# Optimization experiments

Hardware: AMD Instinct MI355X
Metric: run time of the kernel (lower is better)

## Reference

```python
import jax, jax.numpy as jnp
import numpy as np

# Dims derived from module build() with d_model=256
D_MODEL = 256
EXPAND = 2
D_STATE = 16
K_CONV = 4
CHUNK = 64
HEADDIM = 64
D_INNER = EXPAND * D_MODEL            # 512
NHEADS = D_INNER // HEADDIM           # 8
CONV_DIM = D_INNER + 2 * D_STATE      # 544
D_IN_PROJ = 3 * D_INNER + 2 * D_STATE + NHEADS  # 1576
BATCH, SEQ = 4, 4096


def setup_inputs() -> dict:
    key = jax.random.key(0)
    ks = jax.random.split(key, 11)
    def rn(k, shape, s=1.0):
        return jax.random.normal(k, shape, dtype=jnp.float32) * s
    return {
        "x": rn(ks[0], (BATCH, SEQ, D_MODEL)),
        "W_in": rn(ks[1], (D_MODEL, D_IN_PROJ), D_MODEL ** -0.5),
        "conv_w": rn(ks[2], (K_CONV, CONV_DIM), 0.3),
        "conv_b": rn(ks[3], (CONV_DIM,), 0.1),
        "A_log": rn(ks[4], (NHEADS, 2), 0.5),
        "dt_bias": rn(ks[5], (NHEADS,), 0.1),
        "D": rn(ks[6], (2 * NHEADS, 1), 0.5),
        "init_conv_state": rn(ks[7], (1, K_CONV, CONV_DIM), 0.1),
        "init_ssm_state": rn(ks[8], (1, 1, NHEADS, HEADDIM, D_STATE, 2), 0.1),
        "norm_w": rn(ks[9], (2 * D_INNER,), 0.5),
        "W_out": rn(ks[10], (2 * D_INNER, D_MODEL), (2 * D_INNER) ** -0.5),
    }


def _exp_segsum(a):
    # a: (..., T) complex. Returns exp(segsum(a)): lower-triangular (incl. diag)
    # with entry [i,j] = exp(sum_{j<d<=i} a_d), zero strictly above the diagonal.
    T = a.shape[-1]
    cs = jnp.cumsum(a, axis=-1)
    seg = cs[..., :, None] - cs[..., None, :]
    mask = jnp.tril(jnp.ones((T, T), dtype=bool))
    seg = jnp.where(mask, seg, 0.0)  # keep exp finite / grad-safe off-band
    return jnp.where(mask, jnp.exp(seg), 0.0)


def reference(x, W_in, conv_w, conv_b, A_log, dt_bias, D, init_conv_state,
              init_ssm_state, norm_w, W_out):
    b, L, _ = x.shape
    zxbcdt = x @ W_in  # (b, L, 3*d_inner + 2*d_state + nheads)
    z = zxbcdt[..., : 2 * D_INNER]
    xBC = zxbcdt[..., 2 * D_INNER: 3 * D_INNER + 2 * D_STATE]
    dt_raw = zxbcdt[..., 3 * D_INNER + 2 * D_STATE:]
    # dt scalar in call is 1/30, then *30 -> net factor 1
    dt = jnp.clip(jnp.exp(dt_raw + dt_bias), 0.0, 6.0)  # (b, L, h)

    # causal depthwise conv1d with learned initial conv state, relu6 activation
    prefix = jnp.broadcast_to(init_conv_state, (b, K_CONV, CONV_DIM))
    full = jnp.concatenate([prefix, xBC], axis=1)  # (b, K_CONV + L, conv_dim)
    conv = conv_b + sum(conv_w[j] * full[:, 1 + j: 1 + j + L] for j in range(K_CONV))
    xBC = jnp.clip(conv, 0.0, 6.0)  # relu6, last L of the L+1 valid outputs

    xin = xBC[..., :D_INNER]
    Bm = xBC[..., D_INNER: D_INNER + D_STATE].astype(jnp.complex64)
    Cm = xBC[..., D_INNER + D_STATE:].astype(jnp.complex64)
    xh = xin.reshape(b, L, NHEADS, HEADDIM).astype(jnp.complex64)

    A = -jnp.exp(A_log[:, 0]) + 1j * A_log[:, 1]  # (h,) complex
    dtc = dt.astype(jnp.complex64)
    Adt = A * dtc              # (b, L, h)
    xdt = xh * dtc[..., None]  # (b, L, h, p)

    # ---- chunked SSD (Mamba2-style) with complex state ----
    c = L // CHUNK
    xc = xdt.reshape(b, c, CHUNK, NHEADS, HEADDIM)
    Ac = Adt.reshape(b, c, CHUNK, NHEADS).transpose(0, 3, 1, 2)  # (b, h, c, l)
    Bc = Bm.reshape(b, c, CHUNK, D_STATE)
    Cc = Cm.reshape(b, c, CHUNK, D_STATE)

    A_cum = jnp.cumsum(Ac, axis=-1)          # (b, h, c, l)
    Lmat = _exp_segsum(Ac)                   # (b, h, c, l, l)
    Y_diag = jnp.einsum('bcln,bcsn,bhcls,bcshp->bclhp', Cc, Bc, Lmat, xc)

    decay_states = jnp.exp(A_cum[..., -1:] - A_cum)  # (b, h, c, l)
    states = jnp.einsum('bcln,bhcl,bclhp->bchpn', Bc, decay_states, xc)

    init_stat = init_ssm_state[:, 0, ..., 0] + 1j * init_ssm_state[:, 0, ..., 1]
    init_stat = jnp.broadcast_to(init_stat, (b, NHEADS, HEADDIM, D_STATE))[:, None]
    states = jnp.concatenate([init_stat, states], axis=1)  # (b, c+1, h, p, n)

    decay_chunk = _exp_segsum(jnp.pad(A_cum[..., -1], ((0, 0), (0, 0), (1, 0))))
    new_states = jnp.einsum('bhzc,bchpn->bzhpn', decay_chunk, states)
    Y_off = jnp.einsum('bcln,bchpn,bhcl->bclhp', Cc, new_states[:, :-1], jnp.exp(A_cum))

    Y = (Y_diag + Y_off).reshape(b, L, NHEADS, HEADDIM)  # complex

    # 'b l h p c -> b l (h c) p' : interleave real/imag per head
    y2 = jnp.stack([Y.real, Y.imag], axis=3).reshape(b, L, 2 * NHEADS, HEADDIM)
    xr = xin.reshape(b, L, NHEADS, HEADDIM)
    x2 = jnp.stack([xr, jnp.zeros_like(xr)], axis=3).reshape(b, L, 2 * NHEADS, HEADDIM)
    y2 = y2 + x2 * D  # D: (2h, 1) broadcasts over p
    y3 = y2.reshape(b, L, 2 * D_INNER)

    # RMSNorm gated by relu6(z)
    yz = y3 * jnp.clip(z, 0.0, 6.0)
    y4 = yz * jax.lax.rsqrt(jnp.mean(yz * yz, axis=-1, keepdims=True) + 1e-5) * norm_w
    return y4 @ W_out
```

## Files before the change

kernel.cpp:

```cpp
#include <hip/hip_runtime.h>
#include <math.h>

#define BATCHN 4
#define SEQL   4096
#define DMODEL 256
#define DIP    1576
#define DINNER 512
#define DZCOLS 1024
#define CONVD  544
#define NHEADS 8
#define HDIM   64
#define DSTATE 16
#define CHK    64
#define NCHUNK 64
#define MROWS  (BATCHN*SEQL)
#define NPAD   1664

typedef _Float16 half8 __attribute__((ext_vector_type(8)));
typedef short    s16x8 __attribute__((ext_vector_type(8)));
typedef float    f32x4 __attribute__((ext_vector_type(4)));

__device__ __forceinline__ float clip6f(float x) { return fminf(fmaxf(x, 0.0f), 6.0f); }

__global__ __launch_bounds__(256) void k_cvt_x(const float* __restrict__ X,
                                               _Float16* __restrict__ A)
{
    const int gid = blockIdx.x * 256 + threadIdx.x;
    const float4 a = *reinterpret_cast<const float4*>(X + (size_t)gid * 8);
    const float4 b = *reinterpret_cast<const float4*>(X + (size_t)gid * 8 + 4);
    half8 h;
    h[0] = (_Float16)a.x; h[1] = (_Float16)a.y; h[2] = (_Float16)a.z; h[3] = (_Float16)a.w;
    h[4] = (_Float16)b.x; h[5] = (_Float16)b.y; h[6] = (_Float16)b.z; h[7] = (_Float16)b.w;
    *reinterpret_cast<half8*>(A + (size_t)gid * 8) = h;
}

__global__ __launch_bounds__(256) void k_cvt_win(const float* __restrict__ W,
                                                 _Float16* __restrict__ Bt)
{
    const int gid = blockIdx.x * 256 + threadIdx.x;
    const int k = gid & 255, n = gid >> 8;
    const float v = (n < DIP) ? W[(size_t)k * DIP + n] : 0.0f;
    Bt[gid] = (_Float16)v;
}

__global__ __launch_bounds__(256) void k_cvt_wout(const float* __restrict__ W,
                                                  const float* __restrict__ nw,
                                                  _Float16* __restrict__ Bt)
{
    const int gid = blockIdx.x * 256 + threadIdx.x;
    const int k = gid & 1023, n = gid >> 10;
    Bt[gid] = (_Float16)(W[(size_t)k * DMODEL + n] * nw[k]);
}

template<int KTOT, bool NGUARD, bool SCALE>
__global__ __launch_bounds__(256) void k_gemm16(const _Float16* __restrict__ A,
                                                const _Float16* __restrict__ Bt,
                                                float* __restrict__ C,
                                                const int ldc, const int ncols,
                                                const float* __restrict__ scale)
{
    __shared__ _Float16 As[128][72];
    __shared__ _Float16 Bs[128][72];
    const int t  = threadIdx.x;
    const int m0 = blockIdx.y * 128;
    const int n0 = blockIdx.x * 128;
    const int lane = t & 63, wid = t >> 6;
    const int wr = wid >> 1, wc = wid & 1;
    const int fr = lane & 15, fq = lane >> 4;

    f32x4 acc[4][4];
#pragma unroll
    for (int m = 0; m < 4; ++m)
#pragma unroll
        for (int n = 0; n < 4; ++n)
#pragma unroll
            for (int e = 0; e < 4; ++e) acc[m][n][e] = 0.0f;

    for (int kt = 0; kt < KTOT; kt += 64) {
#pragma unroll
        for (int q = 0; q < 4; ++q) {
            const int idx = t + q * 256;
            const int r = idx >> 3, ch = idx & 7;
            *reinterpret_cast<s16x8*>(&As[r][ch * 8]) =
                *reinterpret_cast<const s16x8*>(A + (size_t)(m0 + r) * KTOT + kt + ch * 8);
            *reinterpret_cast<s16x8*>(&Bs[r][ch * 8]) =
                *reinterpret_cast<const s16x8*>(Bt + (size_t)(n0 + r) * KTOT + kt + ch * 8);
        }
        __syncthreads();
#pragma unroll
        for (int ks = 0; ks < 64; ks += 32) {
            half8 af[4], bf[4];
#pragma unroll
            for (int m = 0; m < 4; ++m)
                af[m] = *reinterpret_cast<const half8*>(&As[wr * 64 + m * 16 + fr][ks + fq * 8]);
#pragma unroll
            for (int n = 0; n < 4; ++n)
                bf[n] = *reinterpret_cast<const half8*>(&Bs[wc * 64 + n * 16 + fr][ks + fq * 8]);
#pragma unroll
            for (int m = 0; m < 4; ++m)
#pragma unroll
                for (int n = 0; n < 4; ++n)
                    acc[m][n] = __builtin_amdgcn_mfma_f32_16x16x32_f16(af[m], bf[n], acc[m][n], 0, 0, 0);
        }
        __syncthreads();
    }

#pragma unroll
    for (int m = 0; m < 4; ++m)
#pragma unroll
        for (int j = 0; j < 4; ++j) {
            const int row = m0 + wr * 64 + m * 16 + fq * 4 + j;
            const float sc = SCALE ? scale[row] : 1.0f;
#pragma unroll
            for (int n = 0; n < 4; ++n) {
                const int col = n0 + wc * 64 + n * 16 + fr;
                if (!NGUARD || col < ncols)
                    C[(size_t)row * ldc + col] = acc[m][n][j] * sc;
            }
        }
}

__global__ __launch_bounds__(256) void k_conv(const float* __restrict__ zx,
                                              const float* __restrict__ conv_w,
                                              const float* __restrict__ conv_b,
                                              const float* __restrict__ init_conv,
                                              float* __restrict__ convout)
{
    const int NC4 = CONVD / 4;
    int gid = blockIdx.x * 256 + threadIdx.x;
    if (gid >= MROWS * NC4) return;
    const int row  = gid / NC4;
    const int c    = (gid % NC4) * 4;
    const int b    = row / SEQL;
    const int tpos = row % SEQL;
    float4 acc = *reinterpret_cast<const float4*>(conv_b + c);
#pragma unroll
    for (int j = 0; j < 4; ++j) {
        const int srct = tpos - 3 + j;
        float4 v;
        if (srct >= 0)
            v = *reinterpret_cast<const float4*>(zx + (size_t)(b * SEQL + srct) * DIP + DZCOLS + c);
        else
            v = *reinterpret_cast<const float4*>(init_conv + (size_t)(tpos + 1 + j) * CONVD + c);
        const float4 w = *reinterpret_cast<const float4*>(conv_w + (size_t)j * CONVD + c);
        acc.x = fmaf(w.x, v.x, acc.x);
        acc.y = fmaf(w.y, v.y, acc.y);
        acc.z = fmaf(w.z, v.z, acc.z);
        acc.w = fmaf(w.w, v.w, acc.w);
    }
    acc.x = clip6f(acc.x); acc.y = clip6f(acc.y);
    acc.z = clip6f(acc.z); acc.w = clip6f(acc.w);
    *reinterpret_cast<float4*>(convout + (size_t)row * CONVD + c) = acc;
}

__global__ __launch_bounds__(256) void k_states(const float* __restrict__ zx,
                                                const float* __restrict__ conv,
                                                const float* __restrict__ A_log,
                                                const float* __restrict__ dt_bias,
                                                float* __restrict__ Acum,
                                                float* __restrict__ ctbuf,
                                                float* __restrict__ st)
{
    const int c = blockIdx.x, h = blockIdx.y, b = blockIdx.z;
    __shared__ float wr[CHK], wi[CHK];
    __shared__ float xs[CHK][HDIM];
    __shared__ float Bsh[CHK][DSTATE];
    const int t = threadIdx.x;

#pragma unroll
    for (int q = 0; q < 4; ++q) {
        const int g = t + q * 256;
        const int l = g >> 4, p4 = (g & 15) * 4;
        const float4 v = *reinterpret_cast<const float4*>(
            conv + (size_t)(b * SEQL + c * CHK + l) * CONVD + h * HDIM + p4);
        xs[l][p4 + 0] = v.x; xs[l][p4 + 1] = v.y; xs[l][p4 + 2] = v.z; xs[l][p4 + 3] = v.w;
    }
    {
        const int l = t >> 2, n4 = (t & 3) * 4;
        const float4 v = *reinterpret_cast<const float4*>(
            conv + (size_t)(b * SEQL + c * CHK + l) * CONVD + DINNER + n4);
        Bsh[l][n4 + 0] = v.x; Bsh[l][n4 + 1] = v.y; Bsh[l][n4 + 2] = v.z; Bsh[l][n4 + 3] = v.w;
    }

    if (t < 64) {
        const int l = t;
        const int row = b * SEQL + c * CHK + l;
        const float dtv = fminf(__expf(zx[(size_t)row * DIP + 1568 + h] + dt_bias[h]), 6.0f);
        const float Ar = -__expf(A_log[2 * h]);
        const float Ai = A_log[2 * h + 1];
        float cr = Ar * dtv, ci = Ai * dtv;
#pragma unroll
        for (int off = 1; off < 64; off <<= 1) {
            const float pr = __shfl_up(cr, off);
            const float pi = __shfl_up(ci, off);
            if (l >= off) { cr += pr; ci += pi; }
        }
        const size_t aidx = ((((size_t)b * NHEADS + h) * NCHUNK + c) * CHK + l) * 2;
        Acum[aidx] = cr; Acum[aidx + 1] = ci;
        const float ctr = __shfl(cr, 63), cti = __shfl(ci, 63);
        if (l == 63) {
            const size_t ci2 = (((size_t)b * NHEADS + h) * NCHUNK + c) * 2;
            ctbuf[ci2] = ctr; ctbuf[ci2 + 1] = cti;
        }
        const float e = __expf(ctr - cr);
        float sn, cn; sincosf(cti - ci, &sn, &cn);
        wr[l] = e * cn * dtv;
        wi[l] = e * sn * dtv;
    }
    __syncthreads();

    const int p = t >> 2, n0 = (t & 3) * 4;
    float accr[4] = {0.f, 0.f, 0.f, 0.f};
    float acci[4] = {0.f, 0.f, 0.f, 0.f};
    for (int l = 0; l < CHK; ++l) {
        const float xv = xs[l][p];
        const float xr = xv * wr[l];
        const float xi = xv * wi[l];
#pragma unroll
        for (int j = 0; j < 4; ++j) {
            const float bb = Bsh[l][n0 + j];
            accr[j] = fmaf(bb, xr, accr[j]);
            acci[j] = fmaf(bb, xi, acci[j]);
        }
    }
    const size_t sidx = (((((size_t)b * NCHUNK + c) * NHEADS + h) * HDIM + p) * DSTATE + n0) * 2;
    float4 o0 = make_float4(accr[0], acci[0], accr[1], acci[1]);
    float4 o1 = make_float4(accr[2], acci[2], accr[3], acci[3]);
    *reinterpret_cast<float4*>(st + sidx)     = o0;
    *reinterpret_cast<float4*>(st + sidx + 4) = o1;
}

__global__ __launch_bounds__(1024) void k_scan(const float* __restrict__ ctbuf,
                                               const float* __restrict__ st,
                                               const float* __restrict__ init_ssm,
                                               float* __restrict__ Sin)
{
    const int h = blockIdx.x, b = blockIdx.y;
    __shared__ float Tr[NCHUNK], Ti[NCHUNK];
    const int t = threadIdx.x;
    if (t < NCHUNK) {
        const size_t ci2 = (((size_t)b * NHEADS + h) * NCHUNK + t) * 2;
        const float e = __expf(ctbuf[ci2]);
        float sn, cn; sincosf(ctbuf[ci2 + 1], &sn, &cn);
        Tr[t] = e * cn; Ti[t] = e * sn;
    }
    __syncthreads();
    const int p = t >> 4, n = t & 15;
    const size_t ii = (((size_t)h * HDIM + p) * DSTATE + n) * 2;
    float Sr = init_ssm[ii], Si = init_ssm[ii + 1];
    for (int z = 0; z < NCHUNK; ++z) {
        const size_t idx = (((((size_t)b * NCHUNK + z) * NHEADS + h) * HDIM + p) * DSTATE + n) * 2;
        Sin[idx] = Sr; Sin[idx + 1] = Si;
        const float sr = st[idx], si = st[idx + 1];
        const float tr = Tr[z], ti = Ti[z];
        const float nr = fmaf(tr, Sr, fmaf(-ti, Si, sr));
        const float ni = fmaf(tr, Si, fmaf(ti, Sr, si));
        Sr = nr; Si = ni;
    }
}

__global__ __launch_bounds__(256) void k_yout(const float* __restrict__ conv,
                                              const float* __restrict__ Acum,
                                              const float* __restrict__ Sin,
                                              const float* __restrict__ Dp,
                                              const float* __restrict__ dt_bias,
                                              const float* __restrict__ zx,
                                              _Float16* __restrict__ A2)
{
    const int c = blockIdx.x, h = blockIdx.y, b = blockIdx.z;
    __shared__ _Float16 Csh[64][40];
    __shared__ _Float16 Bsh[64][40];
    __shared__ _Float16 Srs[64][40];
    __shared__ _Float16 Sis[64][40];
    __shared__ _Float16 Xt[64][72];
    __shared__ _Float16 Gr[64][72];
    __shared__ _Float16 Gi[64][72];
    __shared__ float dts[64], cumr[64], sl_[64], cl_[64], Er[64], Ei[64];
    const int t = threadIdx.x;
    const int lane = t & 63, w = t >> 6;
    const int fr = lane & 15, fq = lane >> 4;
    const int rowb = b * SEQL + c * CHK;

    if (t < 64) {
        const int l = t, row = rowb + l;
        dts[l] = fminf(__expf(zx[(size_t)row * DIP + 1568 + h] + dt_bias[h]), 6.0f);
        const size_t aidx = ((((size_t)b * NHEADS + h) * NCHUNK + c) * CHK + l) * 2;
        const float cr = Acum[aidx], ci = Acum[aidx + 1];
        cumr[l] = cr;
        float sn, cn; sincosf(ci, &sn, &cn);
        sl_[l] = sn; cl_[l] = cn;
        const float e = __expf(cr);
        Er[l] = e * cn; Ei[l] = e * sn;
    }
    {
        const int l = t >> 2, n0 = (t & 3) * 4;
        const float* cp = conv + (size_t)(rowb + l) * CONVD + DINNER;
        const float4 bv = *reinterpret_cast<const float4*>(cp + n0);
        const float4 cv = *reinterpret_cast<const float4*>(cp + DSTATE + n0);
        Bsh[l][n0 + 0] = (_Float16)bv.x; Bsh[l][n0 + 1] = (_Float16)bv.y;
        Bsh[l][n0 + 2] = (_Float16)bv.z; Bsh[l][n0 + 3] = (_Float16)bv.w;
        Csh[l][n0 + 0] = (_Float16)cv.x; Csh[l][n0 + 1] = (_Float16)cv.y;
        Csh[l][n0 + 2] = (_Float16)cv.z; Csh[l][n0 + 3] = (_Float16)cv.w;
        const float* sp = Sin + ((((size_t)b * NCHUNK + c) * NHEADS + h) * HDIM + l) * (DSTATE * 2) + n0 * 2;
        const float4 s0 = *reinterpret_cast<const float4*>(sp);
        const float4 s1 = *reinterpret_cast<const float4*>(sp + 4);
        Srs[l][n0 + 0] = (_Float16)s0.x; Sis[l][n0 + 0] = (_Float16)s0.y;
        Srs[l][n0 + 1] = (_Float16)s0.z; Sis[l][n0 + 1] = (_Float16)s0.w;
        Srs[l][n0 + 2] = (_Float16)s1.x; Sis[l][n0 + 2] = (_Float16)s1.y;
        Srs[l][n0 + 3] = (_Float16)s1.z; Sis[l][n0 + 3] = (_Float16)s1.w;
        const int z0 = 16 + (t & 3) * 4;
#pragma unroll
        for (int e = 0; e < 4; ++e) {
            Bsh[l][z0 + e] = (_Float16)0.0f;
            Csh[l][z0 + e] = (_Float16)0.0f;
            Srs[l][z0 + e] = (_Float16)0.0f;
            Sis[l][z0 + e] = (_Float16)0.0f;
        }
    }
    __syncthreads();

#pragma unroll
    for (int q = 0; q < 4; ++q) {
        const int g = t + q * 256;
        const int l = g >> 4, p4 = (g & 15) * 4;
        const float4 v = *reinterpret_cast<const float4*>(
            conv + (size_t)(rowb + l) * CONVD + h * HDIM + p4);
        const float d = dts[l];
        Xt[p4 + 0][l] = (_Float16)(v.x * d);
        Xt[p4 + 1][l] = (_Float16)(v.y * d);
        Xt[p4 + 2][l] = (_Float16)(v.z * d);
        Xt[p4 + 3][l] = (_Float16)(v.w * d);
    }

    const half8 afC = *reinterpret_cast<const half8*>(&Csh[w * 16 + fr][fq * 8]);
    f32x4 cb[4];
#pragma unroll
    for (int nf = 0; nf < 4; ++nf) {
        const half8 bfB = *reinterpret_cast<const half8*>(&Bsh[nf * 16 + fr][fq * 8]);
        f32x4 z = {0.f, 0.f, 0.f, 0.f};
        cb[nf] = __builtin_amdgcn_mfma_f32_16x16x32_f16(afC, bfB, z, 0, 0, 0);
    }
#pragma unroll
    for (int nf = 0; nf < 4; ++nf) {
        const int s = nf * 16 + fr;
        const float crs = cumr[s], sls = sl_[s], cls = cl_[s];
#pragma unroll
        for (int j = 0; j < 4; ++j) {
            const int l = w * 16 + fq * 4 + j;
            const float dr = fminf(cumr[l] - crs, 0.0f);
            const float e = __expf(dr);
            const float cd = cl_[l] * cls + sl_[l] * sls;
            const float sd = sl_[l] * cls - cl_[l] * sls;
            const float ge = (s <= l) ? cb[nf][j] * e : 0.0f;
            Gr[l][s] = (_Float16)(ge * cd);
            Gi[l][s] = (_Float16)(ge * sd);
        }
    }
    __syncthreads();

    f32x4 accr[4], acci[4];
#pragma unroll
    for (int nf = 0; nf < 4; ++nf)
#pragma unroll
        for (int e = 0; e < 4; ++e) { accr[nf][e] = 0.f; acci[nf][e] = 0.f; }
#pragma unroll
    for (int ks = 0; ks < 64; ks += 32) {
        const half8 ar = *reinterpret_cast<const half8*>(&Gr[w * 16 + fr][ks + fq * 8]);
        const half8 ai = *reinterpret_cast<const half8*>(&Gi[w * 16 + fr][ks + fq * 8]);
#pragma unroll
        for (int nf = 0; nf < 4; ++nf) {
            const half8 bx = *reinterpret_cast<const half8*>(&Xt[nf * 16 + fr][ks + fq * 8]);
            accr[nf] = __builtin_amdgcn_mfma_f32_16x16x32_f16(ar, bx, accr[nf], 0, 0, 0);
            acci[nf] = __builtin_amdgcn_mfma_f32_16x16x32_f16(ai, bx, acci[nf], 0, 0, 0);
        }
    }
    f32x4 orr[4], oii[4];
#pragma unroll
    for (int nf = 0; nf < 4; ++nf) {
        const half8 br = *reinterpret_cast<const half8*>(&Srs[nf * 16 + fr][fq * 8]);
        const half8 bi = *reinterpret_cast<const half8*>(&Sis[nf * 16 + fr][fq * 8]);
        f32x4 z = {0.f, 0.f, 0.f, 0.f};
        orr[nf] = __builtin_amdgcn_mfma_f32_16x16x32_f16(afC, br, z, 0, 0, 0);
        oii[nf] = __builtin_amdgcn_mfma_f32_16x16x32_f16(afC, bi, z, 0, 0, 0);
    }

    const float dcoef = Dp[2 * h];
#pragma unroll
    for (int nf = 0; nf < 4; ++nf) {
        const int p = nf * 16 + fr;
#pragma unroll
        for (int j = 0; j < 4; ++j) {
            const int l = w * 16 + fq * 4 + j;
            const int row = rowb + l;
            const float er = Er[l], ei = Ei[l];
            float yr = accr[nf][j] + er * orr[nf][j] - ei * oii[nf][j];
            float yi = acci[nf][j] + er * oii[nf][j] + ei * orr[nf][j];
            const float xinv = conv[(size_t)row * CONVD + h * HDIM + p];
            yr = fmaf(xinv, dcoef, yr);
            const size_t zidx = (size_t)row * DIP + h * 128 + p;
            const size_t aidx2 = (size_t)row * DZCOLS + h * 128 + p;
            A2[aidx2]      = (_Float16)(yr * clip6f(zx[zidx]));
            A2[aidx2 + 64] = (_Float16)(yi * clip6f(zx[zidx + 64]));
        }
    }
}

__global__ __launch_bounds__(256) void k_rms(const _Float16* __restrict__ A2,
                                             float* __restrict__ scale)
{
    const int w = threadIdx.x >> 6, lane = threadIdx.x & 63;
    const int row = blockIdx.x * 4 + w;
    const _Float16* p = A2 + (size_t)row * DZCOLS + lane * 16;
    float ss = 0.f;
#pragma unroll
    for (int q = 0; q < 2; ++q) {
        const half8 h = *reinterpret_cast<const half8*>(p + q * 8);
#pragma unroll
        for (int e = 0; e < 8; ++e) {
            const float v = (float)h[e];
            ss += v * v;
        }
    }
#pragma unroll
    for (int off = 32; off > 0; off >>= 1) ss += __shfl_down(ss, off);
    if (lane == 0) scale[row] = rsqrtf(ss * (1.0f / 1024.0f) + 1e-5f);
}

extern "C" void kernel_launch(void* const* d_in, const int* in_sizes, int n_in,
                              void* d_out, int out_size, void* d_ws, size_t ws_size,
                              hipStream_t stream)
{
    const float* x         = (const float*)d_in[0];
    const float* W_in      = (const float*)d_in[1];
    const float* conv_w    = (const float*)d_in[2];
    const float* conv_b    = (const float*)d_in[3];
    const float* A_log     = (const float*)d_in[4];
    const float* dt_bias   = (const float*)d_in[5];
    const float* Dp        = (const float*)d_in[6];
    const float* init_conv = (const float*)d_in[7];
    const float* init_ssm  = (const float*)d_in[8];
    const float* norm_w    = (const float*)d_in[9];
    const float* W_out     = (const float*)d_in[10];
    float* out = (float*)d_out;

    float* ws      = (float*)d_ws;
    float* zx      = ws;
    float* convout = zx + (size_t)MROWS * DIP;
    float* Acum    = convout + (size_t)MROWS * CONVD;
    float* ctbuf   = Acum + (size_t)BATCHN * NHEADS * NCHUNK * CHK * 2;
    float* stbuf   = ctbuf + (size_t)BATCHN * NHEADS * NCHUNK * 2;
    float* SinBuf  = stbuf + (size_t)BATCHN * NCHUNK * NHEADS * HDIM * DSTATE * 2;
    float* scaleb  = SinBuf + (size_t)BATCHN * NCHUNK * NHEADS * HDIM * DSTATE * 2;
    float* poolf   = scaleb + MROWS;
    _Float16* A16  = (_Float16*)poolf;
    _Float16* Bt16 = A16 + (size_t)MROWS * DMODEL;
    _Float16* A2   = A16;
    _Float16* Wot  = A16 + (size_t)MROWS * DZCOLS;

    k_cvt_x<<<dim3(MROWS * DMODEL / 8 / 256), dim3(256), 0, stream>>>(x, A16);
    k_cvt_win<<<dim3(NPAD), dim3(256), 0, stream>>>(W_in, Bt16);
    k_cvt_wout<<<dim3(DZCOLS), dim3(256), 0, stream>>>(W_out, norm_w, Wot);

    k_gemm16<DMODEL, true, false><<<dim3(NPAD / 128, MROWS / 128), dim3(256), 0, stream>>>(
        A16, Bt16, zx, DIP, DIP, nullptr);

    const int convThreads = MROWS * (CONVD / 4);
    k_conv<<<(convThreads + 255) / 256, dim3(256), 0, stream>>>(zx, conv_w, conv_b, init_conv, convout);

    k_states<<<dim3(NCHUNK, NHEADS, BATCHN), dim3(256), 0, stream>>>(
        zx, convout, A_log, dt_bias, Acum, ctbuf, stbuf);

    k_scan<<<dim3(NHEADS, BATCHN), dim3(1024), 0, stream>>>(ctbuf, stbuf, init_ssm, SinBuf);

    k_yout<<<dim3(NCHUNK, NHEADS, BATCHN), dim3(256), 0, stream>>>(
        convout, Acum, SinBuf, Dp, dt_bias, zx, A2);

    k_rms<<<dim3(MROWS / 4), dim3(256), 0, stream>>>(A2, scaleb);

    k_gemm16<DZCOLS, false, true><<<dim3(DMODEL / 128, MROWS / 128), dim3(256), 0, stream>>>(
        A2, Wot, out, DMODEL, DMODEL, scaleb);
}
```

Measured before the change: 246.4 us.

## Store intermediates in fp16 and fuse x-convert and RMS norm into GEMMs

Intermediate activations (in-proj output and conv output) are now stored as fp16 instead of fp32, with dt_raw kept in a separate small fp32 buffer to preserve precision for the exp. The fp32-to-fp16 conversion of x moves into the input GEMM's tile load. The RMS sum-of-squares moves into the output GEMM's A-tile load, which removes two kernel launches and their extra passes over global memory. Together these are meant to roughly halve intermediate memory traffic. The cost is reduced precision in the conv inputs and outputs and the z gate, and each output-GEMM column block recomputes the row norms.

```diff
diff --git a/kernel.cpp b/kernel.cpp
--- a/kernel.cpp
+++ b/kernel.cpp
@@ -17,22 +17,11 @@
 #define NPAD   1664
 
 typedef _Float16 half8 __attribute__((ext_vector_type(8)));
+typedef _Float16 half4 __attribute__((ext_vector_type(4)));
 typedef short    s16x8 __attribute__((ext_vector_type(8)));
 typedef float    f32x4 __attribute__((ext_vector_type(4)));
 
 __device__ __forceinline__ float clip6f(float x) { return fminf(fmaxf(x, 0.0f), 6.0f); }
-
-__global__ __launch_bounds__(256) void k_cvt_x(const float* __restrict__ X,
-                                               _Float16* __restrict__ A)
-{
-    const int gid = blockIdx.x * 256 + threadIdx.x;
-    const float4 a = *reinterpret_cast<const float4*>(X + (size_t)gid * 8);
-    const float4 b = *reinterpret_cast<const float4*>(X + (size_t)gid * 8 + 4);
-    half8 h;
-    h[0] = (_Float16)a.x; h[1] = (_Float16)a.y; h[2] = (_Float16)a.z; h[3] = (_Float16)a.w;
-    h[4] = (_Float16)b.x; h[5] = (_Float16)b.y; h[6] = (_Float16)b.z; h[7] = (_Float16)b.w;
-    *reinterpret_cast<half8*>(A + (size_t)gid * 8) = h;
-}
 
 __global__ __launch_bounds__(256) void k_cvt_win(const float* __restrict__ W,
                                                  _Float16* __restrict__ Bt)
@@ -52,12 +41,10 @@
     Bt[gid] = (_Float16)(W[(size_t)k * DMODEL + n] * nw[k]);
 }
 
-template<int KTOT, bool NGUARD, bool SCALE>
-__global__ __launch_bounds__(256) void k_gemm16(const _Float16* __restrict__ A,
-                                                const _Float16* __restrict__ Bt,
-                                                float* __restrict__ C,
-                                                const int ldc, const int ncols,
-                                                const float* __restrict__ scale)
+__global__ __launch_bounds__(256) void k_gemm_in(const float* __restrict__ X,
+                                                 const _Float16* __restrict__ Bt,
+                                                 _Float16* __restrict__ zx,
+                                                 float* __restrict__ dtraw)
 {
     __shared__ _Float16 As[128][72];
     __shared__ _Float16 Bs[128][72];
@@ -76,15 +63,22 @@
 #pragma unroll
             for (int e = 0; e < 4; ++e) acc[m][n][e] = 0.0f;
 
-    for (int kt = 0; kt < KTOT; kt += 64) {
+    for (int kt = 0; kt < DMODEL; kt += 64) {
 #pragma unroll
         for (int q = 0; q < 4; ++q) {
             const int idx = t + q * 256;
             const int r = idx >> 3, ch = idx & 7;
-            *reinterpret_cast<s16x8*>(&As[r][ch * 8]) =
-                *reinterpret_cast<const s16x8*>(A + (size_t)(m0 + r) * KTOT + kt + ch * 8);
+            const float* xp = X + (size_t)(m0 + r) * DMODEL + kt + ch * 8;
+            const float4 a0 = *reinterpret_cast<const float4*>(xp);
+            const float4 a1 = *reinterpret_cast<const float4*>(xp + 4);
+            half8 hv;
+            hv[0] = (_Float16)a0.x; hv[1] = (_Float16)a0.y;
+            hv[2] = (_Float16)a0.z; hv[3] = (_Float16)a0.w;
+            hv[4] = (_Float16)a1.x; hv[5] = (_Float16)a1.y;
+            hv[6] = (_Float16)a1.z; hv[7] = (_Float16)a1.w;
+            *reinterpret_cast<half8*>(&As[r][ch * 8]) = hv;
             *reinterpret_cast<s16x8*>(&Bs[r][ch * 8]) =
-                *reinterpret_cast<const s16x8*>(Bt + (size_t)(n0 + r) * KTOT + kt + ch * 8);
+                *reinterpret_cast<const s16x8*>(Bt + (size_t)(n0 + r) * DMODEL + kt + ch * 8);
         }
         __syncthreads();
 #pragma unroll
@@ -110,51 +104,70 @@
 #pragma unroll
         for (int j = 0; j < 4; ++j) {
             const int row = m0 + wr * 64 + m * 16 + fq * 4 + j;
-            const float sc = SCALE ? scale[row] : 1.0f;
 #pragma unroll
             for (int n = 0; n < 4; ++n) {
                 const int col = n0 + wc * 64 + n * 16 + fr;
-                if (!NGUARD || col < ncols)
-                    C[(size_t)row * ldc + col] = acc[m][n][j] * sc;
+                const float v = acc[m][n][j];
+                if (col < DIP) {
+                    zx[(size_t)row * DIP + col] = (_Float16)v;
+                    if (col >= 3 * DINNER + 2 * DSTATE)
+                        dtraw[(size_t)row * 8 + (col - (3 * DINNER + 2 * DSTATE))] = v;
+                }
             }
         }
 }
 
-__global__ __launch_bounds__(256) void k_conv(const float* __restrict__ zx,
+__global__ __launch_bounds__(256) void k_conv(const _Float16* __restrict__ zx,
                                               const float* __restrict__ conv_w,
                                               const float* __restrict__ conv_b,
                                               const float* __restrict__ init_conv,
-                                              float* __restrict__ convout)
-{
-    const int NC4 = CONVD / 4;
-    int gid = blockIdx.x * 256 + threadIdx.x;
-    if (gid >= MROWS * NC4) return;
-    const int row  = gid / NC4;
-    const int c    = (gid % NC4) * 4;
+                                              _Float16* __restrict__ convout)
+{
+    const int NC8 = CONVD / 8;
+    const int gid = blockIdx.x * 256 + threadIdx.x;
+    if (gid >= MROWS * NC8) return;
+    const int row  = gid / NC8;
+    const int c    = (gid % NC8) * 8;
     const int b    = row / SEQL;
     const int tpos = row % SEQL;
-    float4 acc = *reinterpret_cast<const float4*>(conv_b + c);
+    float acc[8];
+    {
+        const float4 b0 = *reinterpret_cast<const float4*>(conv_b + c);
+        const float4 b1 = *reinterpret_cast<const float4*>(conv_b + c + 4);
+        acc[0] = b0.x; acc[1] = b0.y; acc[2] = b0.z; acc[3] = b0.w;
+        acc[4] = b1.x; acc[5] = b1.y; acc[6] = b1.z; acc[7] = b1.w;
+    }
 #pragma unroll
     for (int j = 0; j < 4; ++j) {
         const int srct = tpos - 3 + j;
-        float4 v;
-        if (srct >= 0)
-            v = *reinterpret_cast<const float4*>(zx + (size_t)(b * SEQL + srct) * DIP + DZCOLS + c);
-        else
-            v = *reinterpret_cast<const float4*>(init_conv + (size_t)(tpos + 1 + j) * CONVD + c);
-        const float4 w = *reinterpret_cast<const float4*>(conv_w + (size_t)j * CONVD + c);
-        acc.x = fmaf(w.x, v.x, acc.x);
-        acc.y = fmaf(w.y, v.y, acc.y);
-        acc.z = fmaf(w.z, v.z, acc.z);
-        acc.w = fmaf(w.w, v.w, acc.w);
-    }
-    acc.x = clip6f(acc.x); acc.y = clip6f(acc.y);
-    acc.z = clip6f(acc.z); acc.w = clip6f(acc.w);
-    *reinterpret_cast<float4*>(convout + (size_t)row * CONVD + c) = acc;
-}
-
-__global__ __launch_bounds__(256) void k_states(const float* __restrict__ zx,
-                                                const float* __restrict__ conv,
+        float v[8];
+        if (srct >= 0) {
+            const half8 hv = *reinterpret_cast<const half8*>(
+                zx + (size_t)(b * SEQL + srct) * DIP + DZCOLS + c);
+#pragma unroll
+            for (int e = 0; e < 8; ++e) v[e] = (float)hv[e];
+        } else {
+            const float* ip = init_conv + (size_t)(tpos + 1 + j) * CONVD + c;
+            const float4 i0 = *reinterpret_cast<const float4*>(ip);
+            const float4 i1 = *reinterpret_cast<const float4*>(ip + 4);
+            v[0] = i0.x; v[1] = i0.y; v[2] = i0.z; v[3] = i0.w;
+            v[4] = i1.x; v[5] = i1.y; v[6] = i1.z; v[7] = i1.w;
+        }
+        const float* wp = conv_w + (size_t)j * CONVD + c;
+        const float4 w0 = *reinterpret_cast<const float4*>(wp);
+        const float4 w1 = *reinterpret_cast<const float4*>(wp + 4);
+        const float w[8] = {w0.x, w0.y, w0.z, w0.w, w1.x, w1.y, w1.z, w1.w};
+#pragma unroll
+        for (int e = 0; e < 8; ++e) acc[e] = fmaf(w[e], v[e], acc[e]);
+    }
+    half8 hv;
+#pragma unroll
+    for (int e = 0; e < 8; ++e) hv[e] = (_Float16)clip6f(acc[e]);
+    *reinterpret_cast<half8*>(convout + (size_t)row * CONVD + c) = hv;
+}
+
+__global__ __launch_bounds__(256) void k_states(const float* __restrict__ dtraw,
+                                                const _Float16* __restrict__ conv,
                                                 const float* __restrict__ A_log,
                                                 const float* __restrict__ dt_bias,
                                                 float* __restrict__ Acum,
@@ -168,24 +181,26 @@
     const int t = threadIdx.x;
 
 #pragma unroll
-    for (int q = 0; q < 4; ++q) {
+    for (int q = 0; q < 2; ++q) {
         const int g = t + q * 256;
-        const int l = g >> 4, p4 = (g & 15) * 4;
-        const float4 v = *reinterpret_cast<const float4*>(
-            conv + (size_t)(b * SEQL + c * CHK + l) * CONVD + h * HDIM + p4);
-        xs[l][p4 + 0] = v.x; xs[l][p4 + 1] = v.y; xs[l][p4 + 2] = v.z; xs[l][p4 + 3] = v.w;
-    }
-    {
-        const int l = t >> 2, n4 = (t & 3) * 4;
-        const float4 v = *reinterpret_cast<const float4*>(
-            conv + (size_t)(b * SEQL + c * CHK + l) * CONVD + DINNER + n4);
-        Bsh[l][n4 + 0] = v.x; Bsh[l][n4 + 1] = v.y; Bsh[l][n4 + 2] = v.z; Bsh[l][n4 + 3] = v.w;
+        const int l = g >> 3, p8 = (g & 7) * 8;
+        const half8 hv = *reinterpret_cast<const half8*>(
+            conv + (size_t)(b * SEQL + c * CHK + l) * CONVD + h * HDIM + p8);
+#pragma unroll
+        for (int e = 0; e < 8; ++e) xs[l][p8 + e] = (float)hv[e];
+    }
+    if (t < 128) {
+        const int l = t >> 1, n8 = (t & 1) * 8;
+        const half8 hv = *reinterpret_cast<const half8*>(
+            conv + (size_t)(b * SEQL + c * CHK + l) * CONVD + DINNER + n8);
+#pragma unroll
+        for (int e = 0; e < 8; ++e) Bsh[l][n8 + e] = (float)hv[e];
     }
 
     if (t < 64) {
         const int l = t;
         const int row = b * SEQL + c * CHK + l;
-        const float dtv = fminf(__expf(zx[(size_t)row * DIP + 1568 + h] + dt_bias[h]), 6.0f);
+        const float dtv = fminf(__expf(dtraw[(size_t)row * 8 + h] + dt_bias[h]), 6.0f);
         const float Ar = -__expf(A_log[2 * h]);
         const float Ai = A_log[2 * h + 1];
         float cr = Ar * dtv, ci = Ai * dtv;
@@ -259,12 +274,13 @@
     }
 }
 
-__global__ __launch_bounds__(256) void k_yout(const float* __restrict__ conv,
+__global__ __launch_bounds__(256) void k_yout(const _Float16* __restrict__ conv,
                                               const float* __restrict__ Acum,
                                               const float* __restrict__ Sin,
                                               const float* __restrict__ Dp,
                                               const float* __restrict__ dt_bias,
-                                              const float* __restrict__ zx,
+                                              const float* __restrict__ dtraw,
+                                              const _Float16* __restrict__ zx,
                                               _Float16* __restrict__ A2)
 {
     const int c = blockIdx.x, h = blockIdx.y, b = blockIdx.z;
@@ -283,7 +299,7 @@
 
     if (t < 64) {
         const int l = t, row = rowb + l;
-        dts[l] = fminf(__expf(zx[(size_t)row * DIP + 1568 + h] + dt_bias[h]), 6.0f);
+        dts[l] = fminf(__expf(dtraw[(size_t)row * 8 + h] + dt_bias[h]), 6.0f);
         const size_t aidx = ((((size_t)b * NHEADS + h) * NCHUNK + c) * CHK + l) * 2;
         const float cr = Acum[aidx], ci = Acum[aidx + 1];
         cumr[l] = cr;
@@ -293,21 +309,21 @@
         Er[l] = e * cn; Ei[l] = e * sn;
     }
     {
-        const int l = t >> 2, n0 = (t & 3) * 4;
-        const float* cp = conv + (size_t)(rowb + l) * CONVD + DINNER;
-        const float4 bv = *reinterpret_cast<const float4*>(cp + n0);
-        const float4 cv = *reinterpret_cast<const float4*>(cp + DSTATE + n0);
-        Bsh[l][n0 + 0] = (_Float16)bv.x; Bsh[l][n0 + 1] = (_Float16)bv.y;
-        Bsh[l][n0 + 2] = (_Float16)bv.z; Bsh[l][n0 + 3] = (_Float16)bv.w;
-        Csh[l][n0 + 0] = (_Float16)cv.x; Csh[l][n0 + 1] = (_Float16)cv.y;
-        Csh[l][n0 + 2] = (_Float16)cv.z; Csh[l][n0 + 3] = (_Float16)cv.w;
-        const float* sp = Sin + ((((size_t)b * NCHUNK + c) * NHEADS + h) * HDIM + l) * (DSTATE * 2) + n0 * 2;
+        const int l = t >> 2, n4 = (t & 3) * 4;
+        const _Float16* cp = conv + (size_t)(rowb + l) * CONVD + DINNER;
+        const half4 bv = *reinterpret_cast<const half4*>(cp + n4);
+        const half4 cv = *reinterpret_cast<const half4*>(cp + DSTATE + n4);
+        Bsh[l][n4 + 0] = bv[0]; Bsh[l][n4 + 1] = bv[1];
+        Bsh[l][n4 + 2] = bv[2]; Bsh[l][n4 + 3] = bv[3];
+        Csh[l][n4 + 0] = cv[0]; Csh[l][n4 + 1] = cv[1];
+        Csh[l][n4 + 2] = cv[2]; Csh[l][n4 + 3] = cv[3];
+        const float* sp = Sin + ((((size_t)b * NCHUNK + c) * NHEADS + h) * HDIM + l) * (DSTATE * 2) + n4 * 2;
         const float4 s0 = *reinterpret_cast<const float4*>(sp);
         const float4 s1 = *reinterpret_cast<const float4*>(sp + 4);
-        Srs[l][n0 + 0] = (_Float16)s0.x; Sis[l][n0 + 0] = (_Float16)s0.y;
-        Srs[l][n0 + 1] = (_Float16)s0.z; Sis[l][n0 + 1] = (_Float16)s0.w;
-        Srs[l][n0 + 2] = (_Float16)s1.x; Sis[l][n0 + 2] = (_Float16)s1.y;
-        Srs[l][n0 + 3] = (_Float16)s1.z; Sis[l][n0 + 3] = (_Float16)s1.w;
+        Srs[l][n4 + 0] = (_Float16)s0.x; Sis[l][n4 + 0] = (_Float16)s0.y;
+        Srs[l][n4 + 1] = (_Float16)s0.z; Sis[l][n4 + 1] = (_Float16)s0.w;
+        Srs[l][n4 + 2] = (_Float16)s1.x; Sis[l][n4 + 2] = (_Float16)s1.y;
+        Srs[l][n4 + 3] = (_Float16)s1.z; Sis[l][n4 + 3] = (_Float16)s1.w;
         const int z0 = 16 + (t & 3) * 4;
 #pragma unroll
         for (int e = 0; e < 4; ++e) {
@@ -320,16 +336,15 @@
     __syncthreads();
 
 #pragma unroll
-    for (int q = 0; q < 4; ++q) {
+    for (int q = 0; q < 2; ++q) {
         const int g = t + q * 256;
-        const int l = g >> 4, p4 = (g & 15) * 4;
-        const float4 v = *reinterpret_cast<const float4*>(
-            conv + (size_t)(rowb + l) * CONVD + h * HDIM + p4);
+        const int l = g >> 3, p8 = (g & 7) * 8;
+        const half8 hv = *reinterpret_cast<const half8*>(
+            conv + (size_t)(rowb + l) * CONVD + h * HDIM + p8);
         const float d = dts[l];
-        Xt[p4 + 0][l] = (_Float16)(v.x * d);
-        Xt[p4 + 1][l] = (_Float16)(v.y * d);
-        Xt[p4 + 2][l] = (_Float16)(v.z * d);
-        Xt[p4 + 3][l] = (_Float16)(v.w * d);
+#pragma unroll
+        for (int e = 0; e < 8; ++e)
+            Xt[p8 + e][l] = (_Float16)((float)hv[e] * d);
     }
 
     const half8 afC = *reinterpret_cast<const half8*>(&Csh[w * 16 + fr][fq * 8]);
@@ -395,35 +410,99 @@
             const float er = Er[l], ei = Ei[l];
             float yr = accr[nf][j] + er * orr[nf][j] - ei * oii[nf][j];
             float yi = acci[nf][j] + er * oii[nf][j] + ei * orr[nf][j];
-            const float xinv = conv[(size_t)row * CONVD + h * HDIM + p];
+            const float xinv = (float)conv[(size_t)row * CONVD + h * HDIM + p];
             yr = fmaf(xinv, dcoef, yr);
             const size_t zidx = (size_t)row * DIP + h * 128 + p;
+            const float zr = (float)zx[zidx], zi2 = (float)zx[zidx + 64];
             const size_t aidx2 = (size_t)row * DZCOLS + h * 128 + p;
-            A2[aidx2]      = (_Float16)(yr * clip6f(zx[zidx]));
-            A2[aidx2 + 64] = (_Float16)(yi * clip6f(zx[zidx + 64]));
-        }
-    }
-}
-
-__global__ __launch_bounds__(256) void k_rms(const _Float16* __restrict__ A2,
-                                             float* __restrict__ scale)
-{
-    const int w = threadIdx.x >> 6, lane = threadIdx.x & 63;
-    const int row = blockIdx.x * 4 + w;
-    const _Float16* p = A2 + (size_t)row * DZCOLS + lane * 16;
-    float ss = 0.f;
-#pragma unroll
-    for (int q = 0; q < 2; ++q) {
-        const half8 h = *reinterpret_cast<const half8*>(p + q * 8);
-#pragma unroll
-        for (int e = 0; e < 8; ++e) {
-            const float v = (float)h[e];
-            ss += v * v;
-        }
-    }
-#pragma unroll
-    for (int off = 32; off > 0; off >>= 1) ss += __shfl_down(ss, off);
-    if (lane == 0) scale[row] = rsqrtf(ss * (1.0f / 1024.0f) + 1e-5f);
+            A2[aidx2]      = (_Float16)(yr * clip6f(zr));
+            A2[aidx2 + 64] = (_Float16)(yi * clip6f(zi2));
+        }
+    }
+}
+
+__global__ __launch_bounds__(256) void k_gemm_out(const _Float16* __restrict__ A,
+                                                  const _Float16* __restrict__ Bt,
+                                                  float* __restrict__ C)
+{
+    __shared__ _Float16 As[128][72];
+    __shared__ _Float16 Bs[128][72];
+    __shared__ float ssp[128][8];
+    __shared__ float scl[128];
+    const int t  = threadIdx.x;
+    const int m0 = blockIdx.y * 128;
+    const int n0 = blockIdx.x * 128;
+    const int lane = t & 63, wid = t >> 6;
+    const int wr = wid >> 1, wc = wid & 1;
+    const int fr = lane & 15, fq = lane >> 4;
+
+    f32x4 acc[4][4];
+#pragma unroll
+    for (int m = 0; m < 4; ++m)
+#pragma unroll
+        for (int n = 0; n < 4; ++n)
+#pragma unroll
+            for (int e = 0; e < 4; ++e) acc[m][n][e] = 0.0f;
+    float ss[4] = {0.f, 0.f, 0.f, 0.f};
+
+    for (int kt = 0; kt < DZCOLS; kt += 64) {
+#pragma unroll
+        for (int q = 0; q < 4; ++q) {
+            const int idx = t + q * 256;
+            const int r = idx >> 3, ch = idx & 7;
+            const half8 av = *reinterpret_cast<const half8*>(
+                A + (size_t)(m0 + r) * DZCOLS + kt + ch * 8);
+            *reinterpret_cast<half8*>(&As[r][ch * 8]) = av;
+            float s = 0.f;
+#pragma unroll
+            for (int e = 0; e < 8; ++e) { const float f = (float)av[e]; s = fmaf(f, f, s); }
+            ss[q] += s;
+            *reinterpret_cast<s16x8*>(&Bs[r][ch * 8]) =
+                *reinterpret_cast<const s16x8*>(Bt + (size_t)(n0 + r) * DZCOLS + kt + ch * 8);
+        }
+        __syncthreads();
+#pragma unroll
+        for (int ks = 0; ks < 64; ks += 32) {
+            half8 af[4], bf[4];
+#pragma unroll
+            for (int m = 0; m < 4; ++m)
+                af[m] = *reinterpret_cast<const half8*>(&As[wr * 64 + m * 16 + fr][ks + fq * 8]);
+#pragma unroll
+            for (int n = 0; n < 4; ++n)
+                bf[n] = *reinterpret_cast<const half8*>(&Bs[wc * 64 + n * 16 + fr][ks + fq * 8]);
+#pragma unroll
+            for (int m = 0; m < 4; ++m)
+#pragma unroll
+                for (int n = 0; n < 4; ++n)
+                    acc[m][n] = __builtin_amdgcn_mfma_f32_16x16x32_f16(af[m], bf[n], acc[m][n], 0, 0, 0);
+        }
+        __syncthreads();
+    }
+
+#pragma unroll
+    for (int q = 0; q < 4; ++q) ssp[(t >> 3) + q * 32][t & 7] = ss[q];
+    __syncthreads();
+    if (t < 128) {
+        float s = 0.f;
+#pragma unroll
+        for (int ch = 0; ch < 8; ++ch) s += ssp[t][ch];
+        scl[t] = rsqrtf(s * (1.0f / 1024.0f) + 1e-5f);
+    }
+    __syncthreads();
+
+#pragma unroll
+    for (int m = 0; m < 4; ++m)
+#pragma unroll
+        for (int j = 0; j < 4; ++j) {
+            const int rloc = wr * 64 + m * 16 + fq * 4 + j;
+            const int row = m0 + rloc;
+            const float sc = scl[rloc];
+#pragma unroll
+            for (int n = 0; n < 4; ++n) {
+                const int col = n0 + wc * 64 + n * 16 + fr;
+                C[(size_t)row * DMODEL + col] = acc[m][n][j] * sc;
+            }
+        }
 }
 
 extern "C" void kernel_launch(void* const* d_in, const int* in_sizes, int n_in,
@@ -444,39 +523,35 @@
     float* out = (float*)d_out;
 
     float* ws      = (float*)d_ws;
-    float* zx      = ws;
-    float* convout = zx + (size_t)MROWS * DIP;
-    float* Acum    = convout + (size_t)MROWS * CONVD;
+    float* dtraw   = ws;
+    float* Acum    = dtraw + (size_t)MROWS * 8;
     float* ctbuf   = Acum + (size_t)BATCHN * NHEADS * NCHUNK * CHK * 2;
     float* stbuf   = ctbuf + (size_t)BATCHN * NHEADS * NCHUNK * 2;
     float* SinBuf  = stbuf + (size_t)BATCHN * NCHUNK * NHEADS * HDIM * DSTATE * 2;
-    float* scaleb  = SinBuf + (size_t)BATCHN * NCHUNK * NHEADS * HDIM * DSTATE * 2;
-    float* poolf   = scaleb + MROWS;
-    _Float16* A16  = (_Float16*)poolf;
-    _Float16* Bt16 = A16 + (size_t)MROWS * DMODEL;
-    _Float16* A2   = A16;
-    _Float16* Wot  = A16 + (size_t)MROWS * DZCOLS;
-
-    k_cvt_x<<<dim3(MROWS * DMODEL / 8 / 256), dim3(256), 0, stream>>>(x, A16);
+    _Float16* zx      = (_Float16*)(SinBuf + (size_t)BATCHN * NCHUNK * NHEADS * HDIM * DSTATE * 2);
+    _Float16* convout = zx + (size_t)MROWS * DIP;
+    _Float16* A2      = convout + (size_t)MROWS * CONVD;
+    _Float16* Bt16    = A2 + (size_t)MROWS * DZCOLS;
+    _Float16* Wot     = Bt16 + (size_t)NPAD * DMODEL;
+
     k_cvt_win<<<dim3(NPAD), dim3(256), 0, stream>>>(W_in, Bt16);
     k_cvt_wout<<<dim3(DZCOLS), dim3(256), 0, stream>>>(W_out, norm_w, Wot);
 
-    k_gemm16<DMODEL, true, false><<<dim3(NPAD / 128, MROWS / 128), dim3(256), 0, stream>>>(
-        A16, Bt16, zx, DIP, DIP, nullptr);
-
-    const int convThreads = MROWS * (CONVD / 4);
-    k_conv<<<(convThreads + 255) / 256, dim3(256), 0, stream>>>(zx, conv_w, conv_b, init_conv, convout);
+    k_gemm_in<<<dim3(NPAD / 128, MROWS / 128), dim3(256), 0, stream>>>(
+        x, Bt16, zx, dtraw);
+
+    const int convThreads = MROWS * (CONVD / 8);
+    k_conv<<<(convThreads + 255) / 256, dim3(256), 0, stream>>>(
+        zx, conv_w, conv_b, init_conv, convout);
 
     k_states<<<dim3(NCHUNK, NHEADS, BATCHN), dim3(256), 0, stream>>>(
-        zx, convout, A_log, dt_bias, Acum, ctbuf, stbuf);
+        dtraw, convout, A_log, dt_bias, Acum, ctbuf, stbuf);
 
     k_scan<<<dim3(NHEADS, BATCHN), dim3(1024), 0, stream>>>(ctbuf, stbuf, init_ssm, SinBuf);
 
     k_yout<<<dim3(NCHUNK, NHEADS, BATCHN), dim3(256), 0, stream>>>(
-        convout, Acum, SinBuf, Dp, dt_bias, zx, A2);
-
-    k_rms<<<dim3(MROWS / 4), dim3(256), 0, stream>>>(A2, scaleb);
-
-    k_gemm16<DZCOLS, false, true><<<dim3(DMODEL / 128, MROWS / 128), dim3(256), 0, stream>>>(
-        A2, Wot, out, DMODEL, DMODEL, scaleb);
-}
+        convout, Acum, SinBuf, Dp, dt_bias, dtraw, zx, A2);
+
+    k_gemm_out<<<dim3(DMODEL / 128, MROWS / 128), dim3(256), 0, stream>>>(
+        A2, Wot, out);
+}
```

New measurement: 235.6 us. 4.4% less time.
